# Kernel tuning notes

Hardware: AMD Instinct MI355X
Metric: run time of the kernel (lower is better)

Reference implementation:

```python
import math
import jax, jax.numpy as jnp
import numpy as np


def _skew(X, pad_value):
    # shift every row i one step right relative to row i-1: [B,M,L] -> [B,M,M+L]
    B, M, L = X.shape
    X = jnp.pad(X, ((0, 0), (0, 0), (0, M + 1)), constant_values=pad_value)
    X = X.reshape(B, -1)[:, :-M]
    return X.reshape(B, M, M + L)


def _unskew(X):
    # reverse of _skew: [B,M,M+L] -> [B,M,L]
    B, M, ML = X.shape
    L = ML - M
    X = X.reshape(B, -1)
    X = jnp.pad(X, ((0, 0), (0, M)))
    X = X.reshape(B, M, M + L + 1)
    return X[:, :, :L]


def setup_inputs() -> dict:
    key0 = jax.random.key(0)
    k1, k2, k3, k4 = jax.random.split(key0, 4)
    BH, M, D = 64, 1024, 64          # batch*heads, block len, head dim
    L = 1024                          # attn_span
    return {
        "query": jax.random.normal(k1, (BH, M, D), dtype=jnp.float32),
        "key": jax.random.normal(k2, (BH, M + L, D), dtype=jnp.float32),
        "value": jax.random.normal(k3, (BH, M + L, D), dtype=jnp.float32),
        "key_pe": jax.random.normal(k4, (1, D, L), dtype=jnp.float32),
    }


def reference(query, key, value, key_pe):
    hidden_size = query.shape[-1]
    # content scores: [BH, M, M+L] -> banded [BH, M, L]
    attn_cont = _unskew(jnp.matmul(query, jnp.swapaxes(key, -1, -2)))
    # relative position scores: [BH, M, L] (key_pe broadcasts over batch)
    attn_pos = jnp.matmul(query, key_pe)
    attn = (attn_cont + attn_pos) / math.sqrt(hidden_size)
    attn = jax.nn.softmax(attn, axis=-1)
    # dropout p=0.0 -> identity
    attn_skew = _skew(attn, 0.0)          # [BH, M, M+L]
    out = jnp.matmul(attn_skew, value)    # [BH, M, D]
    return out
```

## Files before the change

kernel.cpp:

```cpp
#include <hip/hip_runtime.h>
#include <hip/hip_bf16.h>


typedef __attribute__((ext_vector_type(8))) short bf16x8;
typedef __attribute__((ext_vector_type(4))) short bf16x4;
typedef __attribute__((ext_vector_type(4))) float f32x4;

#define BHN   64
#define MQ    1024
#define DH    64
#define LS    1024
#define NKEY  2048
#define NTILE 17

#define SZ_PE  ((size_t)LS * DH * 2)
#define OFF_K  SZ_PE
#define SZ_K   ((size_t)BHN * NKEY * DH * 2)
#define OFF_V  (OFF_K + SZ_K)
#define SZ_V   ((size_t)BHN * DH * NKEY * 2)
#define WS_NEED (OFF_V + SZ_V)

#define SCL_LOG2E 0.18033688011112042f

__device__ __forceinline__ short f2bf(float f) {
  unsigned u = __float_as_uint(f);
  u += 0x7FFFu + ((u >> 16) & 1u);
  return (short)(u >> 16);
}
__device__ __forceinline__ float bf2f(short s) {
  return __uint_as_float(((unsigned)(unsigned short)s) << 16);
}
__device__ __forceinline__ unsigned packbf(float a, float b) {
  return (unsigned)(unsigned short)f2bf(a) | ((unsigned)(unsigned short)f2bf(b) << 16);
}
__device__ __forceinline__ void async_copy16(const void* g, void* l) {
  __builtin_amdgcn_global_load_lds((const __attribute__((address_space(1))) void*)g,
                                   (__attribute__((address_space(3))) void*)l, 16, 0, 0);
}

__global__ __launch_bounds__(256)
void prep_fused(const float* __restrict__ pe, const float* __restrict__ K,
                const float* __restrict__ V, short* __restrict__ peT,
                short* __restrict__ Kb, short* __restrict__ Vb) {
  __shared__ short st[64 * 68];
  const int bx = blockIdx.x;
  if (bx < 256) {
    const int idx = bx * 256 + threadIdx.x;
    const int rel = idx >> 6, d = idx & 63;
    peT[rel * 64 + (((d >> 3) ^ (rel & 7)) * 8) + (d & 7)] = f2bf(pe[d * LS + rel]);
  } else if (bx < 2304) {
    const size_t i = ((size_t)(bx - 256) * 256 + threadIdx.x) * 16;
    const int row = (int)(i >> 6);
    const int c16 = (int)(i & 63);
    const float4 f0 = *(const float4*)(K + i);
    const float4 f1 = *(const float4*)(K + i + 4);
    const float4 f2 = *(const float4*)(K + i + 8);
    const float4 f3 = *(const float4*)(K + i + 12);
    bf16x8 b0, b1;
    b0[0]=f2bf(f0.x); b0[1]=f2bf(f0.y); b0[2]=f2bf(f0.z); b0[3]=f2bf(f0.w);
    b0[4]=f2bf(f1.x); b0[5]=f2bf(f1.y); b0[6]=f2bf(f1.z); b0[7]=f2bf(f1.w);
    b1[0]=f2bf(f2.x); b1[1]=f2bf(f2.y); b1[2]=f2bf(f2.z); b1[3]=f2bf(f2.w);
    b1[4]=f2bf(f3.x); b1[5]=f2bf(f3.y); b1[6]=f2bf(f3.z); b1[7]=f2bf(f3.w);
    const int s7 = row & 7;
    short* dst = Kb + (size_t)row * 64;
    *(bf16x8*)&dst[(((c16 >> 3))     ^ s7) * 8] = b0;
    *(bf16x8*)&dst[(((c16 >> 3) + 1) ^ s7) * 8] = b1;
  } else {
    const int b  = bx - 2304;
    const int bh = b >> 5, jt = b & 31;
    {
      const int r = threadIdx.x >> 2, cb = (threadIdx.x & 3) * 16;
      const float* src = V + ((size_t)bh * NKEY + jt * 64 + r) * DH + cb;
#pragma unroll
      for (int c = 0; c < 16; c += 4) {
        float4 f = *(const float4*)(src + c);
        bf16x4 v = {f2bf(f.x), f2bf(f.y), f2bf(f.z), f2bf(f.w)};
        *(bf16x4*)&st[r * 68 + cb + c] = v;
      }
    }
    __syncthreads();
    {
      const int d = threadIdx.x >> 2, kapb = (threadIdx.x & 3) * 16;
      __attribute__((aligned(16))) short tmp[16];
#pragma unroll
      for (int j = 0; j < 16; ++j) {
        const int kap = kapb + j;
        const int k   = (kap & 3) * 16 + (kap >> 2);
        tmp[j] = st[k * 68 + d];
      }
      short* dst = Vb + ((size_t)bh * DH + d) * NKEY + jt * 64 + kapb;
      *(bf16x8*)dst       = *(bf16x8*)&tmp[0];
      *(bf16x8*)(dst + 8) = *(bf16x8*)&tmp[8];
    }
  }
}

template <bool PRECONV>
__global__ __launch_bounds__(256, 4)
void seq_attn_kernel(const float* __restrict__ Qf, const float* __restrict__ Kf,
                     const float* __restrict__ Vf, const short* __restrict__ peT,
                     const short* __restrict__ Kb, const short* __restrict__ Vb,
                     float* __restrict__ Out) {
  __shared__ short sK[64 * 64];
  __shared__ short sPE[2 * 64 * 64];
  __shared__ short sV[64 * 64];
  __shared__ short sPA[64 * 64];

  const int tid  = threadIdx.x;
  const int w    = tid >> 6;
  const int lane = tid & 63;
  const int li   = lane & 15;
  const int quad = lane >> 4;
  const int linear = blockIdx.y * 16 + blockIdx.x;
  const int slot   = linear >> 3;
  const int bh     = (linear & 7) * 8 + (slot >> 4);
  const int i0     = (slot & 15) * 64;
  const int rbase  = w * 16 + quad * 4;

  bf16x8 aq[2];
  {
    const float* qp = Qf + (size_t)((bh * MQ + i0 + w * 16 + li) * DH) + quad * 8;
#pragma unroll
    for (int ks = 0; ks < 2; ++ks) {
      const float4 f0 = *(const float4*)(qp + ks * 32);
      const float4 f1 = *(const float4*)(qp + ks * 32 + 4);
      bf16x8 a;
      a[0] = f2bf(f0.x); a[1] = f2bf(f0.y); a[2] = f2bf(f0.z); a[3] = f2bf(f0.w);
      a[4] = f2bf(f1.x); a[5] = f2bf(f1.y); a[6] = f2bf(f1.z); a[7] = f2bf(f1.w);
      aq[ks] = a;
    }
  }

  float l_i[4] = {0.f, 0.f, 0.f, 0.f};
  f32x4 acco[4];
#pragma unroll
  for (int nt = 0; nt < 4; ++nt) acco[nt] = (f32x4){0.f, 0.f, 0.f, 0.f};

  f32x4 curPw[4];
  f32x4 prevw3;
  prevw3 = (f32x4){0.f, 0.f, 0.f, 0.f};

  for (int t = 0; t < NTILE; ++t) {
    const int j0 = i0 + t * 64;
    __syncthreads();

    if constexpr (PRECONV) {
      {
        const char* gb = (const char*)(Kb + ((size_t)bh * NKEY + j0) * 64);
#pragma unroll
        for (int it = 0; it < 2; ++it) {
          const int c0 = w * 128 + it * 64;
          async_copy16(gb + (size_t)(c0 + lane) * 16, (char*)sK + (size_t)c0 * 16);
        }
      }
      if (t < NTILE - 1) {
        const char* gb = (const char*)(peT + (size_t)t * 64 * 64);
        char* db = (char*)sPE + (size_t)(t & 1) * 8192;
#pragma unroll
        for (int it = 0; it < 2; ++it) {
          const int c0 = w * 128 + it * 64;
          async_copy16(gb + (size_t)(c0 + lane) * 16, db + (size_t)c0 * 16);
        }
      }
      {
#pragma unroll
        for (int it = 0; it < 2; ++it) {
          const int s = w * 128 + it * 64 + lane;
          const int d = s >> 3;
          const int g = (s & 7) ^ (d & 7);
          const short* gp = Vb + ((size_t)bh * DH + d) * NKEY + j0 + g * 8;
          async_copy16(gp, (char*)sV + (size_t)(w * 128 + it * 64) * 16);
        }
      }
    } else {
      {
        const int srow = tid >> 2, l0 = tid & 3, sdb = l0 * 16;
        const float* src = Kf + (size_t)(bh * NKEY + j0 + srow) * DH + sdb;
        const float4 a0 = *(const float4*)(src + 0);
        const float4 a1 = *(const float4*)(src + 4);
        const float4 a2 = *(const float4*)(src + 8);
        const float4 a3 = *(const float4*)(src + 12);
        bf16x8 b0, b1;
        b0[0]=f2bf(a0.x); b0[1]=f2bf(a0.y); b0[2]=f2bf(a0.z); b0[3]=f2bf(a0.w);
        b0[4]=f2bf(a1.x); b0[5]=f2bf(a1.y); b0[6]=f2bf(a1.z); b0[7]=f2bf(a1.w);
        b1[0]=f2bf(a2.x); b1[1]=f2bf(a2.y); b1[2]=f2bf(a2.z); b1[3]=f2bf(a2.w);
        b1[4]=f2bf(a3.x); b1[5]=f2bf(a3.y); b1[6]=f2bf(a3.z); b1[7]=f2bf(a3.w);
        const int s7 = srow & 7;
        *(bf16x8*)&sK[srow * 64 + (((2 * l0)     ^ s7) * 8)] = b0;
        *(bf16x8*)&sK[srow * 64 + (((2 * l0 + 1) ^ s7) * 8)] = b1;
      }
      {
        const int vdb = (tid & 15) * 4, vkb = (tid >> 4) * 4;
        const float* src = Vf + (size_t)(bh * NKEY + j0 + vkb) * DH + vdb;
#pragma unroll
        for (int m = 0; m < 4; ++m) {
          const float4 rr = *(const float4*)(src + m * DH);
          const int k   = vkb + m;
          const int kap = (k & 15) * 4 + (k >> 4);
#pragma unroll
          for (int jj = 0; jj < 4; ++jj) {
            const int d = vdb + jj;
            const float fv = (jj == 0) ? rr.x : (jj == 1) ? rr.y : (jj == 2) ? rr.z : rr.w;
            sV[d * 64 + (((kap >> 3) ^ (d & 7)) * 8) + (kap & 7)] = f2bf(fv);
          }
        }
      }
      if (t < NTILE - 1) {
        const short* src = peT + (size_t)t * 64 * 64;
        short* db = sPE + (size_t)(t & 1) * 4096;
        *(bf16x8*)&db[tid * 16]     = *(const bf16x8*)(src + tid * 16);
        *(bf16x8*)&db[tid * 16 + 8] = *(const bf16x8*)(src + tid * 16 + 8);
      }
    }
    __syncthreads();

#pragma unroll
    for (int m = 0; m < 4; ++m) {
      const int colIdx = 4 * t - w + m;
      const int base = ((colIdx >> 2) & 1) * 4096 + ((colIdx & 3) * 16 + li) * 64;
      f32x4 c = (f32x4){0.f, 0.f, 0.f, 0.f};
#pragma unroll
      for (int ks = 0; ks < 2; ++ks) {
        const int gs = (((ks * 4 + quad) ^ (li & 7)) * 8);
        const bf16x8 b = *(bf16x8*)&sPE[base + gs];
        c = __builtin_amdgcn_mfma_f32_16x16x32_bf16(aq[ks], b, c, 0, 0, 0);
      }
      curPw[m] = c;
    }

    f32x4 cs[4];
#pragma unroll
    for (int nt = 0; nt < 4; ++nt) {
      f32x4 c = (f32x4){0.f, 0.f, 0.f, 0.f};
#pragma unroll
      for (int ks = 0; ks < 2; ++ks) {
        const int gs = (((ks * 4 + quad) ^ (li & 7)) * 8);
        const bf16x8 b = *(bf16x8*)&sK[(nt * 16 + li) * 64 + gs];
        c = __builtin_amdgcn_mfma_f32_16x16x32_bf16(aq[ks], b, c, 0, 0, 0);
      }
      cs[nt] = c;
    }

#pragma unroll
    for (int r = 0; r < 4; ++r) {
      const int e       = li - quad * 4 - r;
      const bool ge     = (e >= 0);
      const int srcLane = quad * 16 + (e & 15);
      const float shm = __shfl(prevw3[r], srcLane);
      const unsigned pk01 = packbf(curPw[0][r], curPw[1][r]);
      const unsigned pk23 = packbf(curPw[2][r], curPw[3][r]);
      const unsigned s01 = (unsigned)__shfl((int)pk01, srcLane);
      const unsigned s23 = (unsigned)__shfl((int)pk23, srcLane);
      const float sh0 = bf2f((short)(s01 & 0xffffu));
      const float sh1 = bf2f((short)(s01 >> 16));
      const float sh2 = bf2f((short)(s23 & 0xffffu));
      const float sh3 = bf2f((short)(s23 >> 16));
      const float pos0 = ge ? sh0 : shm;
      const float pos1 = ge ? sh1 : sh0;
      const float pos2 = ge ? sh2 : sh1;
      const float pos3 = ge ? sh3 : sh2;
      float p0 = __builtin_exp2f((cs[0][r] + pos0) * SCL_LOG2E);
      float p1 = __builtin_exp2f((cs[1][r] + pos1) * SCL_LOG2E);
      float p2 = __builtin_exp2f((cs[2][r] + pos2) * SCL_LOG2E);
      float p3 = __builtin_exp2f((cs[3][r] + pos3) * SCL_LOG2E);
      if (t == 0) {
        p0 = (0 > w || (0 == w && ge)) ? p0 : 0.f;
        p1 = (1 > w || (1 == w && ge)) ? p1 : 0.f;
        p2 = (2 > w || (2 == w && ge)) ? p2 : 0.f;
        p3 = (3 > w || (3 == w && ge)) ? p3 : 0.f;
      } else if (t == NTILE - 1) {
        p0 = (0 < w || (0 == w && !ge)) ? p0 : 0.f;
        p1 = (1 < w || (1 == w && !ge)) ? p1 : 0.f;
        p2 = (2 < w || (2 == w && !ge)) ? p2 : 0.f;
        p3 = (3 < w || (3 == w && !ge)) ? p3 : 0.f;
      }
      l_i[r] += (p0 + p1) + (p2 + p3);
      const int rowA = rbase + r;
      const bf16x4 pk = {f2bf(p0), f2bf(p1), f2bf(p2), f2bf(p3)};
      *(bf16x4*)&sPA[rowA * 64 + (((li >> 1) ^ (rowA & 7)) * 8) + (li & 1) * 4] = pk;
    }
    prevw3 = curPw[3];

#pragma unroll
    for (int ks = 0; ks < 2; ++ks) {
      const int rowA = w * 16 + li;
      const bf16x8 ap =
          *(bf16x8*)&sPA[rowA * 64 + (((ks * 4 + quad) ^ (rowA & 7)) * 8)];
#pragma unroll
      for (int nt = 0; nt < 4; ++nt) {
        const int d  = nt * 16 + li;
        const int gs = (((ks * 4 + quad) ^ (d & 7)) * 8);
        const bf16x8 bv = *(bf16x8*)&sV[d * 64 + gs];
        acco[nt] = __builtin_amdgcn_mfma_f32_16x16x32_bf16(ap, bv, acco[nt], 0, 0, 0);
      }
    }
  }

#pragma unroll
  for (int r = 0; r < 4; ++r) {
    float l = l_i[r];
    l += __shfl_xor(l, 1);
    l += __shfl_xor(l, 2);
    l += __shfl_xor(l, 4);
    l += __shfl_xor(l, 8);
    const float inv = 1.0f / l;
#pragma unroll
    for (int nt = 0; nt < 4; ++nt) {
      Out[(size_t)(bh * MQ + i0 + rbase + r) * DH + nt * 16 + li] = acco[nt][r] * inv;
    }
  }
}

extern "C" void kernel_launch(void* const* d_in, const int* in_sizes, int n_in,
                              void* d_out, int out_size, void* d_ws, size_t ws_size,
                              hipStream_t stream) {
  const float* q  = (const float*)d_in[0];
  const float* k  = (const float*)d_in[1];
  const float* v  = (const float*)d_in[2];
  const float* pe = (const float*)d_in[3];
  float* out = (float*)d_out;
  short* peT = (short*)d_ws;
  short* Kb  = (short*)((char*)d_ws + OFF_K);
  short* Vb  = (short*)((char*)d_ws + OFF_V);
  const bool preconv = ws_size >= WS_NEED;

  dim3 grid(MQ / 64, BHN);
  if (preconv) {
    prep_fused<<<4352, 256, 0, stream>>>(pe, k, v, peT, Kb, Vb);
    seq_attn_kernel<true><<<grid, 256, 0, stream>>>(q, k, v, peT, Kb, Vb, out);
  } else {
    prep_fused<<<256, 256, 0, stream>>>(pe, k, v, peT, Kb, Vb);
    seq_attn_kernel<false><<<grid, 256, 0, stream>>>(q, k, v, peT, Kb, Vb, out);
  }
}
```

Baseline: 178.0 us.

## Register-prefetch next tiles, fold softmax scale into Q, use packed bf16 converts

Replaces the async global-to-LDS copies with register prefetch: the next tile's K, V and PE fragments are loaded into registers while the current tile is computed, then written to LDS after the barrier. It folds the softmax scale and log2e into the Q conversion so each exp2 no longer needs a multiply. It uses the hardware packed bf16 conversion builtin when available and swaps __syncthreads for a custom waitcnt-plus-barrier. The prefetch adds register pressure, and scaling Q before rounding to bf16 slightly changes numerics.

Measured after the change: 181.9 us. 1.02x slower.

```diff
diff --git a/kernel.cpp b/kernel.cpp
--- a/kernel.cpp
+++ b/kernel.cpp
@@ -30,12 +30,39 @@
 __device__ __forceinline__ float bf2f(short s) {
   return __uint_as_float(((unsigned)(unsigned short)s) << 16);
 }
-__device__ __forceinline__ unsigned packbf(float a, float b) {
+
+#if defined(__has_builtin)
+#if __has_builtin(__builtin_amdgcn_cvt_pk_bf16_f32)
+#define HAVE_CVT_PK 1
+#endif
+#endif
+
+__device__ __forceinline__ unsigned pk2(float a, float b) {
+#ifdef HAVE_CVT_PK
+  auto r = __builtin_amdgcn_cvt_pk_bf16_f32(a, b);
+  unsigned u;
+  __builtin_memcpy(&u, &r, 4);
+  return u;
+#else
   return (unsigned)(unsigned short)f2bf(a) | ((unsigned)(unsigned short)f2bf(b) << 16);
-}
-__device__ __forceinline__ void async_copy16(const void* g, void* l) {
-  __builtin_amdgcn_global_load_lds((const __attribute__((address_space(1))) void*)g,
-                                   (__attribute__((address_space(3))) void*)l, 16, 0, 0);
+#endif
+}
+__device__ __forceinline__ bf16x4 mk4(unsigned a, unsigned b) {
+  union { unsigned u[2]; bf16x4 v; } z;
+  z.u[0] = a; z.u[1] = b;
+  return z.v;
+}
+__device__ __forceinline__ bf16x8 mk8(unsigned a, unsigned b, unsigned c, unsigned d) {
+  union { unsigned u[4]; bf16x8 v; } z;
+  z.u[0] = a; z.u[1] = b; z.u[2] = c; z.u[3] = d;
+  return z.v;
+}
+
+__device__ __forceinline__ void wg_barrier() {
+  __asm__ volatile("" ::: "memory");
+  __builtin_amdgcn_s_waitcnt(0xC07F);
+  __builtin_amdgcn_s_barrier();
+  __asm__ volatile("" ::: "memory");
 }
 
 __global__ __launch_bounds__(256)
@@ -56,11 +83,8 @@
     const float4 f1 = *(const float4*)(K + i + 4);
     const float4 f2 = *(const float4*)(K + i + 8);
     const float4 f3 = *(const float4*)(K + i + 12);
-    bf16x8 b0, b1;
-    b0[0]=f2bf(f0.x); b0[1]=f2bf(f0.y); b0[2]=f2bf(f0.z); b0[3]=f2bf(f0.w);
-    b0[4]=f2bf(f1.x); b0[5]=f2bf(f1.y); b0[6]=f2bf(f1.z); b0[7]=f2bf(f1.w);
-    b1[0]=f2bf(f2.x); b1[1]=f2bf(f2.y); b1[2]=f2bf(f2.z); b1[3]=f2bf(f2.w);
-    b1[4]=f2bf(f3.x); b1[5]=f2bf(f3.y); b1[6]=f2bf(f3.z); b1[7]=f2bf(f3.w);
+    const bf16x8 b0 = mk8(pk2(f0.x, f0.y), pk2(f0.z, f0.w), pk2(f1.x, f1.y), pk2(f1.z, f1.w));
+    const bf16x8 b1 = mk8(pk2(f2.x, f2.y), pk2(f2.z, f2.w), pk2(f3.x, f3.y), pk2(f3.z, f3.w));
     const int s7 = row & 7;
     short* dst = Kb + (size_t)row * 64;
     *(bf16x8*)&dst[(((c16 >> 3))     ^ s7) * 8] = b0;
@@ -72,10 +96,11 @@
       const int r = threadIdx.x >> 2, cb = (threadIdx.x & 3) * 16;
       const float* src = V + ((size_t)bh * NKEY + jt * 64 + r) * DH + cb;
 #pragma unroll
-      for (int c = 0; c < 16; c += 4) {
-        float4 f = *(const float4*)(src + c);
-        bf16x4 v = {f2bf(f.x), f2bf(f.y), f2bf(f.z), f2bf(f.w)};
-        *(bf16x4*)&st[r * 68 + cb + c] = v;
+      for (int c = 0; c < 16; c += 8) {
+        float4 f0 = *(const float4*)(src + c);
+        float4 f1 = *(const float4*)(src + c + 4);
+        *(bf16x8*)&st[r * 68 + cb + c] =
+            mk8(pk2(f0.x, f0.y), pk2(f0.z, f0.w), pk2(f1.x, f1.y), pk2(f1.z, f1.w));
       }
     }
     __syncthreads();
@@ -122,12 +147,11 @@
     const float* qp = Qf + (size_t)((bh * MQ + i0 + w * 16 + li) * DH) + quad * 8;
 #pragma unroll
     for (int ks = 0; ks < 2; ++ks) {
-      const float4 f0 = *(const float4*)(qp + ks * 32);
-      const float4 f1 = *(const float4*)(qp + ks * 32 + 4);
-      bf16x8 a;
-      a[0] = f2bf(f0.x); a[1] = f2bf(f0.y); a[2] = f2bf(f0.z); a[3] = f2bf(f0.w);
-      a[4] = f2bf(f1.x); a[5] = f2bf(f1.y); a[6] = f2bf(f1.z); a[7] = f2bf(f1.w);
-      aq[ks] = a;
+      float4 f0 = *(const float4*)(qp + ks * 32);
+      float4 f1 = *(const float4*)(qp + ks * 32 + 4);
+      f0.x *= SCL_LOG2E; f0.y *= SCL_LOG2E; f0.z *= SCL_LOG2E; f0.w *= SCL_LOG2E;
+      f1.x *= SCL_LOG2E; f1.y *= SCL_LOG2E; f1.z *= SCL_LOG2E; f1.w *= SCL_LOG2E;
+      aq[ks] = mk8(pk2(f0.x, f0.y), pk2(f0.z, f0.w), pk2(f1.x, f1.y), pk2(f1.z, f1.w));
     }
   }
 
@@ -137,40 +161,48 @@
   for (int nt = 0; nt < 4; ++nt) acco[nt] = (f32x4){0.f, 0.f, 0.f, 0.f};
 
   f32x4 curPw[4];
-  f32x4 prevw3;
-  prevw3 = (f32x4){0.f, 0.f, 0.f, 0.f};
+  f32x4 prevw3 = (f32x4){0.f, 0.f, 0.f, 0.f};
+
+  const int slot0 = w * 128 + lane;
+  short* wrK  = sK  + slot0 * 8;
+  short* wrV  = sV  + slot0 * 8;
+  short* wrP0 = sPE + slot0 * 8;
+  short* wrP1 = sPE + 4096 + slot0 * 8;
+  const int vs0d = slot0 >> 3, vs0g = (slot0 & 7) ^ (vs0d & 7);
+  const int s1 = slot0 + 64;
+  const int vs1d = s1 >> 3,  vs1g = (s1 & 7) ^ (vs1d & 7);
+  const short* gK  = Kb + ((size_t)bh * NKEY + i0) * 64 + slot0 * 8;
+  const short* gV0 = Vb + ((size_t)bh * DH + vs0d) * NKEY + i0 + vs0g * 8;
+  const short* gV1 = Vb + ((size_t)bh * DH + vs1d) * NKEY + i0 + vs1g * 8;
+  const short* gPE = peT + slot0 * 8;
+
+  bf16x8 kpf0, kpf1, vpf0, vpf1, ppf0, ppf1;
+  if constexpr (PRECONV) {
+    kpf0 = *(const bf16x8*)gK;  kpf1 = *(const bf16x8*)(gK + 512);  gK += 4096;
+    vpf0 = *(const bf16x8*)gV0; vpf1 = *(const bf16x8*)gV1;  gV0 += 64; gV1 += 64;
+    ppf0 = *(const bf16x8*)gPE; ppf1 = *(const bf16x8*)(gPE + 512); gPE += 4096;
+  }
 
   for (int t = 0; t < NTILE; ++t) {
     const int j0 = i0 + t * 64;
-    __syncthreads();
+    wg_barrier();
 
     if constexpr (PRECONV) {
-      {
-        const char* gb = (const char*)(Kb + ((size_t)bh * NKEY + j0) * 64);
-#pragma unroll
-        for (int it = 0; it < 2; ++it) {
-          const int c0 = w * 128 + it * 64;
-          async_copy16(gb + (size_t)(c0 + lane) * 16, (char*)sK + (size_t)c0 * 16);
-        }
-      }
+      *(bf16x8*)wrK         = kpf0;
+      *(bf16x8*)(wrK + 512) = kpf1;
+      *(bf16x8*)wrV         = vpf0;
+      *(bf16x8*)(wrV + 512) = vpf1;
       if (t < NTILE - 1) {
-        const char* gb = (const char*)(peT + (size_t)t * 64 * 64);
-        char* db = (char*)sPE + (size_t)(t & 1) * 8192;
-#pragma unroll
-        for (int it = 0; it < 2; ++it) {
-          const int c0 = w * 128 + it * 64;
-          async_copy16(gb + (size_t)(c0 + lane) * 16, db + (size_t)c0 * 16);
-        }
-      }
-      {
-#pragma unroll
-        for (int it = 0; it < 2; ++it) {
-          const int s = w * 128 + it * 64 + lane;
-          const int d = s >> 3;
-          const int g = (s & 7) ^ (d & 7);
-          const short* gp = Vb + ((size_t)bh * DH + d) * NKEY + j0 + g * 8;
-          async_copy16(gp, (char*)sV + (size_t)(w * 128 + it * 64) * 16);
-        }
+        short* wp = (t & 1) ? wrP1 : wrP0;
+        *(bf16x8*)wp         = ppf0;
+        *(bf16x8*)(wp + 512) = ppf1;
+      }
+      if (t + 1 < NTILE) {
+        kpf0 = *(const bf16x8*)gK;  kpf1 = *(const bf16x8*)(gK + 512);  gK += 4096;
+        vpf0 = *(const bf16x8*)gV0; vpf1 = *(const bf16x8*)gV1;  gV0 += 64; gV1 += 64;
+      }
+      if (t + 1 < NTILE - 1) {
+        ppf0 = *(const bf16x8*)gPE; ppf1 = *(const bf16x8*)(gPE + 512); gPE += 4096;
       }
     } else {
       {
@@ -180,11 +212,8 @@
         const float4 a1 = *(const float4*)(src + 4);
         const float4 a2 = *(const float4*)(src + 8);
         const float4 a3 = *(const float4*)(src + 12);
-        bf16x8 b0, b1;
-        b0[0]=f2bf(a0.x); b0[1]=f2bf(a0.y); b0[2]=f2bf(a0.z); b0[3]=f2bf(a0.w);
-        b0[4]=f2bf(a1.x); b0[5]=f2bf(a1.y); b0[6]=f2bf(a1.z); b0[7]=f2bf(a1.w);
-        b1[0]=f2bf(a2.x); b1[1]=f2bf(a2.y); b1[2]=f2bf(a2.z); b1[3]=f2bf(a2.w);
-        b1[4]=f2bf(a3.x); b1[5]=f2bf(a3.y); b1[6]=f2bf(a3.z); b1[7]=f2bf(a3.w);
+        const bf16x8 b0 = mk8(pk2(a0.x, a0.y), pk2(a0.z, a0.w), pk2(a1.x, a1.y), pk2(a1.z, a1.w));
+        const bf16x8 b1 = mk8(pk2(a2.x, a2.y), pk2(a2.z, a2.w), pk2(a3.x, a3.y), pk2(a3.z, a3.w));
         const int s7 = srow & 7;
         *(bf16x8*)&sK[srow * 64 + (((2 * l0)     ^ s7) * 8)] = b0;
         *(bf16x8*)&sK[srow * 64 + (((2 * l0 + 1) ^ s7) * 8)] = b1;
@@ -212,7 +241,7 @@
         *(bf16x8*)&db[tid * 16 + 8] = *(const bf16x8*)(src + tid * 16 + 8);
       }
     }
-    __syncthreads();
+    wg_barrier();
 
 #pragma unroll
     for (int m = 0; m < 4; ++m) {
@@ -247,8 +276,8 @@
       const bool ge     = (e >= 0);
       const int srcLane = quad * 16 + (e & 15);
       const float shm = __shfl(prevw3[r], srcLane);
-      const unsigned pk01 = packbf(curPw[0][r], curPw[1][r]);
-      const unsigned pk23 = packbf(curPw[2][r], curPw[3][r]);
+      const unsigned pk01 = pk2(curPw[0][r], curPw[1][r]);
+      const unsigned pk23 = pk2(curPw[2][r], curPw[3][r]);
       const unsigned s01 = (unsigned)__shfl((int)pk01, srcLane);
       const unsigned s23 = (unsigned)__shfl((int)pk23, srcLane);
       const float sh0 = bf2f((short)(s01 & 0xffffu));
@@ -259,10 +288,10 @@
       const float pos1 = ge ? sh1 : sh0;
       const float pos2 = ge ? sh2 : sh1;
       const float pos3 = ge ? sh3 : sh2;
-      float p0 = __builtin_exp2f((cs[0][r] + pos0) * SCL_LOG2E);
-      float p1 = __builtin_exp2f((cs[1][r] + pos1) * SCL_LOG2E);
-      float p2 = __builtin_exp2f((cs[2][r] + pos2) * SCL_LOG2E);
-      float p3 = __builtin_exp2f((cs[3][r] + pos3) * SCL_LOG2E);
+      float p0 = __builtin_exp2f(cs[0][r] + pos0);
+      float p1 = __builtin_exp2f(cs[1][r] + pos1);
+      float p2 = __builtin_exp2f(cs[2][r] + pos2);
+      float p3 = __builtin_exp2f(cs[3][r] + pos3);
       if (t == 0) {
         p0 = (0 > w || (0 == w && ge)) ? p0 : 0.f;
         p1 = (1 > w || (1 == w && ge)) ? p1 : 0.f;
@@ -276,8 +305,8 @@
       }
       l_i[r] += (p0 + p1) + (p2 + p3);
       const int rowA = rbase + r;
-      const bf16x4 pk = {f2bf(p0), f2bf(p1), f2bf(p2), f2bf(p3)};
-      *(bf16x4*)&sPA[rowA * 64 + (((li >> 1) ^ (rowA & 7)) * 8) + (li & 1) * 4] = pk;
+      const bf16x4 pkv = mk4(pk2(p0, p1), pk2(p2, p3));
+      *(bf16x4*)&sPA[rowA * 64 + (((li >> 1) ^ (rowA & 7)) * 8) + (li & 1) * 4] = pkv;
     }
     prevw3 = curPw[3];
 
```
